# Performance work log

Measured on AMD Instinct MI355X. Metric: run time of the kernel, lower is better.

The kernel has to match this reference:

```python
import jax, jax.numpy as jnp
import numpy as np

N = 50000      # nodes
E = 800000     # edges (avg degree 16)
F_IN = 128     # input features
HID = 64       # hidden per head
HEADS = 4      # heads per layer
G = 256        # graphs in batch
C = 10         # classes
ALPHA = 0.01   # leaky relu negative slope


def setup_inputs() -> dict:
    key = jax.random.key(0)
    ks = jax.random.split(key, 12)
    x = jax.random.normal(ks[0], (N, F_IN), dtype=jnp.float32)
    edge_index = jax.random.randint(ks[1], (2, E), 0, N, dtype=jnp.int32)
    batch = jnp.sort(jax.random.randint(ks[2], (N,), 0, G, dtype=jnp.int32))

    def glorot(k, shape):
        fan_in = shape[0] if len(shape) == 2 else int(np.prod(shape[1:]))
        return (jax.random.normal(k, shape, dtype=jnp.float32) / np.float32(np.sqrt(fan_in)))

    W1 = glorot(ks[3], (F_IN, HEADS * HID))
    a1_src = glorot(ks[4], (HEADS, HID))
    a1_dst = glorot(ks[5], (HEADS, HID))
    W2 = glorot(ks[6], (HEADS * HID, HEADS * HID))
    a2_src = glorot(ks[7], (HEADS, HID))
    a2_dst = glorot(ks[8], (HEADS, HID))
    lin_W = glorot(ks[9], (2 * HEADS * HID, C))
    lin_b = jnp.zeros((C,), dtype=jnp.float32)
    return {
        "x": x, "edge_index": edge_index, "batch": batch,
        "W1": W1, "a1_src": a1_src, "a1_dst": a1_dst,
        "W2": W2, "a2_src": a2_src, "a2_dst": a2_dst,
        "lin_W": lin_W, "lin_b": lin_b,
    }


def _gat_layer(x, src, dst, W, a_src, a_dst):
    """Multi-head GAT layer: edge softmax over incoming neighbors, concat heads, ELU."""
    n = x.shape[0]
    h, f = a_src.shape
    Wh = (x @ W).reshape(n, h, f)                       # [N,H,F]
    # per-node attention logits (decomposed GAT attention a^T [Wh_i || Wh_j])
    ls = jnp.einsum("nhf,hf->nh", Wh, a_src)            # [N,H]
    ld = jnp.einsum("nhf,hf->nh", Wh, a_dst)            # [N,H]
    e = jax.nn.leaky_relu(ls[src] + ld[dst], ALPHA)      # [E,H]
    # numerically-stable softmax over edges grouped by destination node
    m = jax.ops.segment_max(e, dst, num_segments=n)      # [N,H]
    m = jnp.where(jnp.isfinite(m), m, 0.0)
    p = jnp.exp(e - m[dst])                              # [E,H]
    z = jax.ops.segment_sum(p, dst, num_segments=n)      # [N,H]
    attn = p / (z[dst] + 1e-16)                          # [E,H]
    msg = Wh[src] * attn[:, :, None]                     # [E,H,F]
    out = jax.ops.segment_sum(msg, dst, num_segments=n)  # [N,H,F]
    return jax.nn.elu(out.reshape(n, h * f))


def reference(x, edge_index, batch, W1, a1_src, a1_dst, W2, a2_src, a2_dst, lin_W, lin_b):
    src, dst = edge_index[0], edge_index[1]
    x = _gat_layer(x, src, dst, W1, a1_src, a1_dst)
    x = _gat_layer(x, src, dst, W2, a2_src, a2_dst)
    # global max / mean pool per graph
    mx = jax.ops.segment_max(x, batch, num_segments=G)
    mx = jnp.where(jnp.isfinite(mx), mx, 0.0)
    s = jax.ops.segment_sum(x, batch, num_segments=G)
    cnt = jax.ops.segment_sum(jnp.ones((x.shape[0], 1), x.dtype), batch, num_segments=G)
    mean = s / jnp.maximum(cnt, 1.0)
    pooled = jnp.concatenate([mx, mean], axis=1)         # [G, 2*H*F]
    return pooled @ lin_W + lin_b                        # [G, C]
```

## Files before the change

kernel.cpp:

```cpp
#include <hip/hip_runtime.h>
#include <hip/hip_bf16.h>

#define NNODES 50000
#define NEDGES 800000
#define FIN    128
#define HID    64
#define HEADS  4
#define NGRAPH 256
#define NCLS   10
#define DTOT   256
#define ALPHA  0.01f
#define CAPLG  6
#define CAP    (1 << CAPLG)

typedef short bf16x8 __attribute__((ext_vector_type(8)));
typedef float f32x4  __attribute__((ext_vector_type(4)));

#define NB      ((NNODES + 255) / 256)
#define EB      ((NEDGES + 255) / 256)
#define XB      ((NNODES * FIN / 4 + 255) / 256)
#define W1B     (FIN * DTOT / 256)
#define W2B     (DTOT * DTOT / 256)

__device__ __forceinline__ ushort f2bf(float v) {
    return __bfloat16_as_ushort(__float2bfloat16(v));
}
__device__ __forceinline__ float blo(unsigned u) { return __uint_as_float(u << 16); }
__device__ __forceinline__ float bhi(unsigned u) { return __uint_as_float(u & 0xffff0000u); }

__global__ __launch_bounds__(256) void k_setup(const int* __restrict__ src, const int* __restrict__ dst,
                                               int* __restrict__ cursor, ushort* __restrict__ esrc,
                                               const int* __restrict__ batch, int* __restrict__ gstart,
                                               const float4* __restrict__ x4, ushort4* __restrict__ xbf4,
                                               const float* __restrict__ W1, ushort* __restrict__ W1t,
                                               const float* __restrict__ W2, ushort* __restrict__ W2t) {
    int b = blockIdx.x, t = threadIdx.x;
    if (b < EB) {
        int e = b * 256 + t;
        if (e < NEDGES) {
            int d = dst[e];
            int pos = atomicAdd(&cursor[d], 1);
            if (pos < CAP) esrc[(d << CAPLG) + pos] = (ushort)src[e];
        }
    } else if (b < EB + NB) {
        int i = (b - EB) * 256 + t;
        if (i >= NNODES) return;
        int bb = batch[i];
        if (i == 0) {
            for (int g = 0; g <= bb; ++g) gstart[g] = 0;
        } else {
            int pb = batch[i - 1];
            if (pb != bb) for (int g = pb + 1; g <= bb; ++g) gstart[g] = i;
        }
        if (i == NNODES - 1)
            for (int g = bb + 1; g <= NGRAPH; ++g) gstart[g] = NNODES;
    } else if (b < EB + NB + XB) {
        int i = (b - EB - NB) * 256 + t;
        if (i >= NNODES * FIN / 4) return;
        float4 v = x4[i];
        ushort4 o;
        o.x = f2bf(v.x); o.y = f2bf(v.y); o.z = f2bf(v.z); o.w = f2bf(v.w);
        xbf4[i] = o;
    } else if (b < EB + NB + XB + W1B) {
        int id = (b - EB - NB - XB) * 256 + t;
        int n = id & 255, k = id >> 8;
        W1t[n * FIN + (((k >> 3) ^ (n & 7)) << 3) + (k & 7)] = f2bf(W1[k * DTOT + n]);
    } else {
        int id = (b - EB - NB - XB - W1B) * 256 + t;
        int n = id & 255, k = id >> 8;
        W2t[n * DTOT + (((k >> 3) ^ (n & 7)) << 3) + (k & 7)] = f2bf(W2[k * DTOT + n]);
    }
}

template <int K>
__global__ __launch_bounds__(256) void k_gemm_mfma(const ushort* __restrict__ Abf,
                                                   const ushort* __restrict__ Bt,
                                                   ushort* __restrict__ Cbf,
                                                   float* __restrict__ ls,
                                                   float* __restrict__ ld_,
                                                   const float* __restrict__ a_src,
                                                   const float* __restrict__ a_dst,
                                                   int M) {
    __shared__ ushort Bl[128 * K];
    const int tid  = threadIdx.x;
    const int w    = tid >> 6;
    const int lane = tid & 63;
    const int l15  = lane & 15;
    const int quad = lane >> 4;
    const int m0 = blockIdx.y * 128;
    const int n0 = blockIdx.x * 128;
    const int hb = blockIdx.x * 2;

    {
        const uint4* sp = (const uint4*)(Bt + (size_t)n0 * K);
        uint4* dp = (uint4*)Bl;
#pragma unroll
        for (int idx = tid; idx < 128 * K / 8; idx += 256) dp[idx] = sp[idx];
    }
    __syncthreads();

    f32x4 acc[2][8];
#pragma unroll
    for (int mf = 0; mf < 2; ++mf)
#pragma unroll
        for (int nf = 0; nf < 8; ++nf)
            acc[mf][nf] = (f32x4){0.f, 0.f, 0.f, 0.f};

    const int rbase = m0 + w * 32;
    int rowA0 = rbase + l15;       if (rowA0 >= M) rowA0 = M - 1;
    int rowA1 = rbase + 16 + l15;  if (rowA1 >= M) rowA1 = M - 1;
    const ushort* pa0 = Abf + (size_t)rowA0 * K + quad * 8;
    const ushort* pa1 = Abf + (size_t)rowA1 * K + quad * 8;

#pragma unroll
    for (int ks = 0; ks < K / 32; ++ks) {
        bf16x8 a0 = *(const bf16x8*)(pa0 + ks * 32);
        bf16x8 a1 = *(const bf16x8*)(pa1 + ks * 32);
        bf16x8 bfr[8];
#pragma unroll
        for (int nf = 0; nf < 8; ++nf) {
            int n = nf * 16 + l15;
            int c = (ks * 4 + quad) ^ (n & 7);
            bfr[nf] = *(const bf16x8*)&Bl[n * K + (c << 3)];
        }
#pragma unroll
        for (int nf = 0; nf < 8; ++nf) {
            acc[0][nf] = __builtin_amdgcn_mfma_f32_16x16x32_bf16(a0, bfr[nf], acc[0][nf], 0, 0, 0);
            acc[1][nf] = __builtin_amdgcn_mfma_f32_16x16x32_bf16(a1, bfr[nf], acc[1][nf], 0, 0, 0);
        }
    }

    float as[8], ad[8];
#pragma unroll
    for (int nf = 0; nf < 8; ++nf) {
        int head = hb + (nf >> 2);
        as[nf] = a_src[head * HID + (nf & 3) * 16 + l15];
        ad[nf] = a_dst[head * HID + (nf & 3) * 16 + l15];
    }
#pragma unroll
    for (int mf = 0; mf < 2; ++mf) {
#pragma unroll
        for (int reg = 0; reg < 4; ++reg) {
            int row = rbase + mf * 16 + quad * 4 + reg;
            bool ok = row < M;
            if (ok) {
#pragma unroll
                for (int nf = 0; nf < 8; ++nf)
                    Cbf[(size_t)row * DTOT + n0 + nf * 16 + l15] = f2bf(acc[mf][nf][reg]);
            }
            float s0 = 0.f, d0 = 0.f, s1 = 0.f, d1 = 0.f;
#pragma unroll
            for (int nf = 0; nf < 4; ++nf) {
                s0 += acc[mf][nf][reg] * as[nf];
                d0 += acc[mf][nf][reg] * ad[nf];
                s1 += acc[mf][nf + 4][reg] * as[nf + 4];
                d1 += acc[mf][nf + 4][reg] * ad[nf + 4];
            }
#pragma unroll
            for (int off = 1; off < 16; off <<= 1) {
                s0 += __shfl_xor(s0, off);
                d0 += __shfl_xor(d0, off);
                s1 += __shfl_xor(s1, off);
                d1 += __shfl_xor(d1, off);
            }
            if (ok && l15 == 0) {
                ls[row * HEADS + hb]      = s0;
                ld_[row * HEADS + hb]     = d0;
                ls[row * HEADS + hb + 1]  = s1;
                ld_[row * HEADS + hb + 1] = d1;
            }
        }
    }
}

__global__ __launch_bounds__(256) void k_gat_aggr(const int* __restrict__ cnt,
                                                  const ushort* __restrict__ esrc,
                                                  const ushort* __restrict__ Whbf,
                                                  const float* __restrict__ ls,
                                                  const float* __restrict__ ld_,
                                                  ushort* __restrict__ out) {
    const int wv   = threadIdx.x >> 6;
    const int lane = threadIdx.x & 63;
    const int i    = blockIdx.x * 4 + wv;
    if (i >= NNODES) return;
    const int half = lane >> 5;
    const int l32  = lane & 31;
    const int h    = l32 >> 3;
    const int e0 = i << CAPLG;
    int deg = cnt[i]; if (deg > CAP) deg = CAP;
    const int e1 = e0 + deg;
    const float ldv = ld_[i * HEADS + h];

    float mx = -INFINITY;
    for (int e = e0 + (l32 & 7) + 8 * half; e < e1; e += 16)
        mx = fmaxf(mx, ls[(int)esrc[e] * HEADS + h]);
    mx = fmaxf(mx, __shfl_xor(mx, 1));
    mx = fmaxf(mx, __shfl_xor(mx, 2));
    mx = fmaxf(mx, __shfl_xor(mx, 4));
    mx = fmaxf(mx, __shfl_xor(mx, 32));
    float lvm = mx + ldv;
    const float M = lvm > 0.f ? lvm : ALPHA * lvm;

    float ac[8] = {};
    float z = 0.f;
    const int ch = 8 * l32;
    int e = e0 + half;
    for (; e + 6 < e1; e += 8) {
        int s0 = (int)esrc[e], s1 = (int)esrc[e + 2], s2 = (int)esrc[e + 4], s3 = (int)esrc[e + 6];
        float l0 = ls[s0 * HEADS + h] + ldv;
        float l1 = ls[s1 * HEADS + h] + ldv;
        float l2 = ls[s2 * HEADS + h] + ldv;
        float l3 = ls[s3 * HEADS + h] + ldv;
        uint4 u0 = *(const uint4*)&Whbf[(size_t)s0 * DTOT + ch];
        uint4 u1 = *(const uint4*)&Whbf[(size_t)s1 * DTOT + ch];
        uint4 u2 = *(const uint4*)&Whbf[(size_t)s2 * DTOT + ch];
        uint4 u3 = *(const uint4*)&Whbf[(size_t)s3 * DTOT + ch];
        float p0 = __expf((l0 > 0.f ? l0 : ALPHA * l0) - M);
        float p1 = __expf((l1 > 0.f ? l1 : ALPHA * l1) - M);
        float p2 = __expf((l2 > 0.f ? l2 : ALPHA * l2) - M);
        float p3 = __expf((l3 > 0.f ? l3 : ALPHA * l3) - M);
        z += p0 + p1 + p2 + p3;
        ac[0] = fmaf(p0, blo(u0.x), ac[0]); ac[1] = fmaf(p0, bhi(u0.x), ac[1]);
        ac[2] = fmaf(p0, blo(u0.y), ac[2]); ac[3] = fmaf(p0, bhi(u0.y), ac[3]);
        ac[4] = fmaf(p0, blo(u0.z), ac[4]); ac[5] = fmaf(p0, bhi(u0.z), ac[5]);
        ac[6] = fmaf(p0, blo(u0.w), ac[6]); ac[7] = fmaf(p0, bhi(u0.w), ac[7]);
        ac[0] = fmaf(p1, blo(u1.x), ac[0]); ac[1] = fmaf(p1, bhi(u1.x), ac[1]);
        ac[2] = fmaf(p1, blo(u1.y), ac[2]); ac[3] = fmaf(p1, bhi(u1.y), ac[3]);
        ac[4] = fmaf(p1, blo(u1.z), ac[4]); ac[5] = fmaf(p1, bhi(u1.z), ac[5]);
        ac[6] = fmaf(p1, blo(u1.w), ac[6]); ac[7] = fmaf(p1, bhi(u1.w), ac[7]);
        ac[0] = fmaf(p2, blo(u2.x), ac[0]); ac[1] = fmaf(p2, bhi(u2.x), ac[1]);
        ac[2] = fmaf(p2, blo(u2.y), ac[2]); ac[3] = fmaf(p2, bhi(u2.y), ac[3]);
        ac[4] = fmaf(p2, blo(u2.z), ac[4]); ac[5] = fmaf(p2, bhi(u2.z), ac[5]);
        ac[6] = fmaf(p2, blo(u2.w), ac[6]); ac[7] = fmaf(p2, bhi(u2.w), ac[7]);
        ac[0] = fmaf(p3, blo(u3.x), ac[0]); ac[1] = fmaf(p3, bhi(u3.x), ac[1]);
        ac[2] = fmaf(p3, blo(u3.y), ac[2]); ac[3] = fmaf(p3, bhi(u3.y), ac[3]);
        ac[4] = fmaf(p3, blo(u3.z), ac[4]); ac[5] = fmaf(p3, bhi(u3.z), ac[5]);
        ac[6] = fmaf(p3, blo(u3.w), ac[6]); ac[7] = fmaf(p3, bhi(u3.w), ac[7]);
    }
    for (; e < e1; e += 2) {
        int s0 = (int)esrc[e];
        float l0 = ls[s0 * HEADS + h] + ldv;
        uint4 u0 = *(const uint4*)&Whbf[(size_t)s0 * DTOT + ch];
        float p0 = __expf((l0 > 0.f ? l0 : ALPHA * l0) - M);
        z += p0;
        ac[0] = fmaf(p0, blo(u0.x), ac[0]); ac[1] = fmaf(p0, bhi(u0.x), ac[1]);
        ac[2] = fmaf(p0, blo(u0.y), ac[2]); ac[3] = fmaf(p0, bhi(u0.y), ac[3]);
        ac[4] = fmaf(p0, blo(u0.z), ac[4]); ac[5] = fmaf(p0, bhi(u0.z), ac[5]);
        ac[6] = fmaf(p0, blo(u0.w), ac[6]); ac[7] = fmaf(p0, bhi(u0.w), ac[7]);
    }

#pragma unroll
    for (int j = 0; j < 8; ++j) ac[j] += __shfl_xor(ac[j], 32);
    z += __shfl_xor(z, 32);

    if (half == 0) {
        const float inv = 1.f / (z + 1e-16f);
        float v[8];
#pragma unroll
        for (int j = 0; j < 8; ++j) {
            float t = ac[j] * inv;
            v[j] = t > 0.f ? t : __expf(t) - 1.f;
        }
        ushort4 pk, pk2;
        pk.x  = f2bf(v[0]); pk.y  = f2bf(v[1]); pk.z  = f2bf(v[2]); pk.w  = f2bf(v[3]);
        pk2.x = f2bf(v[4]); pk2.y = f2bf(v[5]); pk2.z = f2bf(v[6]); pk2.w = f2bf(v[7]);
        *(ushort4*)(out + (size_t)i * DTOT + ch)     = pk;
        *(ushort4*)(out + (size_t)i * DTOT + ch + 4) = pk2;
    }
}

__global__ __launch_bounds__(1024) void k_pool_final(const ushort* __restrict__ h2bf,
                                                     const int* __restrict__ gstart,
                                                     const float* __restrict__ W,
                                                     const float* __restrict__ b,
                                                     float* __restrict__ out) {
    __shared__ float smx[4][256];
    __shared__ float ssm[4][256];
    __shared__ float pooled[2 * DTOT];
    int g = blockIdx.x, t = threadIdx.x;
    int c = t & 255, j = t >> 8;
    int s = gstart[g], e = gstart[g + 1];
    float mx = -INFINITY, sm = 0.f;
    for (int n = s + j; n < e; n += 4) {
        float vv = __uint_as_float(((unsigned)h2bf[(size_t)n * DTOT + c]) << 16);
        mx = fmaxf(mx, vv);
        sm += vv;
    }
    smx[j][c] = mx;
    ssm[j][c] = sm;
    __syncthreads();
    if (t < 256) {
        float m = fmaxf(fmaxf(smx[0][t], smx[1][t]), fmaxf(smx[2][t], smx[3][t]));
        float su = ssm[0][t] + ssm[1][t] + ssm[2][t] + ssm[3][t];
        int cnt = e - s;
        if (cnt <= 0) m = 0.f;
        pooled[t] = m;
        pooled[DTOT + t] = su / (float)(cnt > 0 ? cnt : 1);
    }
    __syncthreads();
    int wv = t >> 6, lane = t & 63;
    if (wv < NCLS) {
        float acc = 0.f;
        for (int k = lane; k < 2 * DTOT; k += 64)
            acc += pooled[k] * W[k * NCLS + wv];
#pragma unroll
        for (int off = 32; off; off >>= 1) acc += __shfl_down(acc, off);
        if (lane == 0)
            out[g * NCLS + wv] = acc + b[wv];
    }
}

extern "C" void kernel_launch(void* const* d_in, const int* in_sizes, int n_in,
                              void* d_out, int out_size, void* d_ws, size_t ws_size,
                              hipStream_t stream) {
    const float* x     = (const float*)d_in[0];
    const int*   ei    = (const int*)d_in[1];
    const int*   batch = (const int*)d_in[2];
    const float* W1    = (const float*)d_in[3];
    const float* a1s   = (const float*)d_in[4];
    const float* a1d   = (const float*)d_in[5];
    const float* W2    = (const float*)d_in[6];
    const float* a2s   = (const float*)d_in[7];
    const float* a2d   = (const float*)d_in[8];
    const float* linW  = (const float*)d_in[9];
    const float* linb  = (const float*)d_in[10];
    float* out = (float*)d_out;

    const int* src = ei;
    const int* dst = ei + NEDGES;

    size_t off = 0;
    char* base = (char*)d_ws;
    auto alloc = [&](size_t bytes) -> void* {
        void* p = base + off;
        off += (bytes + 255) & ~(size_t)255;
        return p;
    };
    ushort* xbf    = (ushort*)alloc((size_t)NNODES * FIN * 2);
    ushort* Whbf   = (ushort*)alloc((size_t)NNODES * DTOT * 2);
    ushort* h1bf   = (ushort*)alloc((size_t)NNODES * DTOT * 2);
    ushort* h2bf   = (ushort*)alloc((size_t)NNODES * DTOT * 2);
    float*  ls     = (float*)alloc((size_t)NNODES * HEADS * 4);
    float*  ld_    = (float*)alloc((size_t)NNODES * HEADS * 4);
    int*    cursor = (int*)alloc((size_t)NNODES * 4);
    ushort* esrc   = (ushort*)alloc((size_t)(NNODES << CAPLG) * 2);
    int*    gstart = (int*)alloc((size_t)(NGRAPH + 1) * 4);
    ushort* W1t    = (ushort*)alloc((size_t)DTOT * FIN * 2);
    ushort* W2t    = (ushort*)alloc((size_t)DTOT * DTOT * 2);

    hipMemsetAsync(cursor, 0, (size_t)NNODES * 4, stream);

    int setup_blocks = EB + NB + XB + W1B + W2B;
    k_setup<<<setup_blocks, 256, 0, stream>>>(src, dst, cursor, esrc, batch, gstart,
                                              (const float4*)x, (ushort4*)xbf,
                                              W1, W1t, W2, W2t);

    dim3 ggrid(2, (NNODES + 127) / 128);

    k_gemm_mfma<FIN><<<ggrid, 256, 0, stream>>>(xbf, W1t, Whbf, ls, ld_, a1s, a1d, NNODES);
    k_gat_aggr<<<(NNODES + 3) / 4, 256, 0, stream>>>(cursor, esrc, Whbf, ls, ld_, h1bf);

    k_gemm_mfma<DTOT><<<ggrid, 256, 0, stream>>>(h1bf, W2t, Whbf, ls, ld_, a2s, a2d, NNODES);
    k_gat_aggr<<<(NNODES + 3) / 4, 256, 0, stream>>>(cursor, esrc, Whbf, ls, ld_, h2bf);

    k_pool_final<<<NGRAPH, 1024, 0, stream>>>(h2bf, gstart, linW, linb, out);
}
```

Baseline: 320.9 us.

## Compute edge softmax once per lane in LDS and use packed FMA aggregation

The GAT aggregation kernel now has each lane own one incoming edge. Each lane computes the logits for all four heads, and wave shuffles give the max and the sum. The normalized attention weights and source ids go into LDS, which removes the separate max pass and the repeated exp and ls gathers in the main loop. The accumulation uses two-wide float FMAs meant to map to packed FMA instructions, and the output is written as a single 16-byte store. The change adds an early exit for zero-degree nodes and relies on the degree cap equalling the wave size.

New measurement: 324.5 us. Within noise of the previous version (+1.1%).

```diff
diff --git a/kernel.cpp b/kernel.cpp
--- a/kernel.cpp
+++ b/kernel.cpp
@@ -15,6 +15,7 @@
 
 typedef short bf16x8 __attribute__((ext_vector_type(8)));
 typedef float f32x4  __attribute__((ext_vector_type(4)));
+typedef float f32x2  __attribute__((ext_vector_type(2)));
 
 #define NB      ((NNODES + 255) / 256)
 #define EB      ((NEDGES + 255) / 256)
@@ -27,6 +28,12 @@
 }
 __device__ __forceinline__ float blo(unsigned u) { return __uint_as_float(u << 16); }
 __device__ __forceinline__ float bhi(unsigned u) { return __uint_as_float(u & 0xffff0000u); }
+__device__ __forceinline__ f32x2 bfpair(unsigned u) {
+    return (f32x2){__uint_as_float(u << 16), __uint_as_float(u & 0xffff0000u)};
+}
+__device__ __forceinline__ unsigned pack2(float lo, float hi) {
+    return ((unsigned)f2bf(hi) << 16) | (unsigned)f2bf(lo);
+}
 
 __global__ __launch_bounds__(256) void k_setup(const int* __restrict__ src, const int* __restrict__ dst,
                                                int* __restrict__ cursor, ushort* __restrict__ esrc,
@@ -179,6 +186,8 @@
                                                   const float* __restrict__ ls,
                                                   const float* __restrict__ ld_,
                                                   ushort* __restrict__ out) {
+    __shared__ float lds_p[4][CAP][HEADS];
+    __shared__ int   lds_s[4][CAP];
     const int wv   = threadIdx.x >> 6;
     const int lane = threadIdx.x & 63;
     const int i    = blockIdx.x * 4 + wv;
@@ -186,86 +195,123 @@
     const int half = lane >> 5;
     const int l32  = lane & 31;
     const int h    = l32 >> 3;
+    const int ch   = 8 * l32;
+
+    int deg = cnt[i]; if (deg > CAP) deg = CAP;
+
+    if (deg == 0) {
+        if (half == 0) {
+            uint4 zz = {0u, 0u, 0u, 0u};
+            *(uint4*)(out + (size_t)i * DTOT + ch) = zz;
+        }
+        return;
+    }
+
     const int e0 = i << CAPLG;
-    int deg = cnt[i]; if (deg > CAP) deg = CAP;
-    const int e1 = e0 + deg;
-    const float ldv = ld_[i * HEADS + h];
-
-    float mx = -INFINITY;
-    for (int e = e0 + (l32 & 7) + 8 * half; e < e1; e += 16)
-        mx = fmaxf(mx, ls[(int)esrc[e] * HEADS + h]);
-    mx = fmaxf(mx, __shfl_xor(mx, 1));
-    mx = fmaxf(mx, __shfl_xor(mx, 2));
-    mx = fmaxf(mx, __shfl_xor(mx, 4));
-    mx = fmaxf(mx, __shfl_xor(mx, 32));
-    float lvm = mx + ldv;
-    const float M = lvm > 0.f ? lvm : ALPHA * lvm;
-
-    float ac[8] = {};
-    float z = 0.f;
-    const int ch = 8 * l32;
-    int e = e0 + half;
-    for (; e + 6 < e1; e += 8) {
-        int s0 = (int)esrc[e], s1 = (int)esrc[e + 2], s2 = (int)esrc[e + 4], s3 = (int)esrc[e + 6];
-        float l0 = ls[s0 * HEADS + h] + ldv;
-        float l1 = ls[s1 * HEADS + h] + ldv;
-        float l2 = ls[s2 * HEADS + h] + ldv;
-        float l3 = ls[s3 * HEADS + h] + ldv;
+    const bool valid = lane < deg;
+    const int  el = valid ? lane : deg - 1;
+    const int  s  = (int)esrc[e0 + el];
+    const float4 ls4 = *(const float4*)(ls + s * HEADS);
+    const float4 ld4 = *(const float4*)(ld_ + (size_t)i * HEADS);
+
+    float eh[4], mh[4];
+#pragma unroll
+    for (int hh = 0; hh < 4; ++hh) {
+        float v = (&ls4.x)[hh] + (&ld4.x)[hh];
+        v = v > 0.f ? v : ALPHA * v;
+        eh[hh] = valid ? v : -INFINITY;
+        mh[hh] = eh[hh];
+    }
+    for (int off = 1; off < deg; off <<= 1) {
+#pragma unroll
+        for (int hh = 0; hh < 4; ++hh)
+            mh[hh] = fmaxf(mh[hh], __shfl_xor(mh[hh], off));
+    }
+    float ph[4], zh[4];
+#pragma unroll
+    for (int hh = 0; hh < 4; ++hh) {
+        ph[hh] = valid ? __expf(eh[hh] - mh[hh]) : 0.f;
+        zh[hh] = ph[hh];
+    }
+    for (int off = 1; off < deg; off <<= 1) {
+#pragma unroll
+        for (int hh = 0; hh < 4; ++hh)
+            zh[hh] += __shfl_xor(zh[hh], off);
+    }
+#pragma unroll
+    for (int hh = 0; hh < 4; ++hh)
+        ph[hh] *= 1.f / (zh[hh] + 1e-16f);
+
+    *(float4*)&lds_p[wv][lane][0] = make_float4(ph[0], ph[1], ph[2], ph[3]);
+    lds_s[wv][lane] = s;
+
+    f32x2 ac[4];
+#pragma unroll
+    for (int j = 0; j < 4; ++j) ac[j] = (f32x2){0.f, 0.f};
+
+    int e = half;
+    for (; e + 6 < deg; e += 8) {
+        int s0 = lds_s[wv][e];
+        int s1 = lds_s[wv][e + 2];
+        int s2 = lds_s[wv][e + 4];
+        int s3 = lds_s[wv][e + 6];
+        float p0 = lds_p[wv][e][h];
+        float p1 = lds_p[wv][e + 2][h];
+        float p2 = lds_p[wv][e + 4][h];
+        float p3 = lds_p[wv][e + 6][h];
         uint4 u0 = *(const uint4*)&Whbf[(size_t)s0 * DTOT + ch];
         uint4 u1 = *(const uint4*)&Whbf[(size_t)s1 * DTOT + ch];
         uint4 u2 = *(const uint4*)&Whbf[(size_t)s2 * DTOT + ch];
         uint4 u3 = *(const uint4*)&Whbf[(size_t)s3 * DTOT + ch];
-        float p0 = __expf((l0 > 0.f ? l0 : ALPHA * l0) - M);
-        float p1 = __expf((l1 > 0.f ? l1 : ALPHA * l1) - M);
-        float p2 = __expf((l2 > 0.f ? l2 : ALPHA * l2) - M);
-        float p3 = __expf((l3 > 0.f ? l3 : ALPHA * l3) - M);
-        z += p0 + p1 + p2 + p3;
-        ac[0] = fmaf(p0, blo(u0.x), ac[0]); ac[1] = fmaf(p0, bhi(u0.x), ac[1]);
-        ac[2] = fmaf(p0, blo(u0.y), ac[2]); ac[3] = fmaf(p0, bhi(u0.y), ac[3]);
-        ac[4] = fmaf(p0, blo(u0.z), ac[4]); ac[5] = fmaf(p0, bhi(u0.z), ac[5]);
-        ac[6] = fmaf(p0, blo(u0.w), ac[6]); ac[7] = fmaf(p0, bhi(u0.w), ac[7]);
-        ac[0] = fmaf(p1, blo(u1.x), ac[0]); ac[1] = fmaf(p1, bhi(u1.x), ac[1]);
-        ac[2] = fmaf(p1, blo(u1.y), ac[2]); ac[3] = fmaf(p1, bhi(u1.y), ac[3]);
-        ac[4] = fmaf(p1, blo(u1.z), ac[4]); ac[5] = fmaf(p1, bhi(u1.z), ac[5]);
-        ac[6] = fmaf(p1, blo(u1.w), ac[6]); ac[7] = fmaf(p1, bhi(u1.w), ac[7]);
-        ac[0] = fmaf(p2, blo(u2.x), ac[0]); ac[1] = fmaf(p2, bhi(u2.x), ac[1]);
-        ac[2] = fmaf(p2, blo(u2.y), ac[2]); ac[3] = fmaf(p2, bhi(u2.y), ac[3]);
-        ac[4] = fmaf(p2, blo(u2.z), ac[4]); ac[5] = fmaf(p2, bhi(u2.z), ac[5]);
-        ac[6] = fmaf(p2, blo(u2.w), ac[6]); ac[7] = fmaf(p2, bhi(u2.w), ac[7]);
-        ac[0] = fmaf(p3, blo(u3.x), ac[0]); ac[1] = fmaf(p3, bhi(u3.x), ac[1]);
-        ac[2] = fmaf(p3, blo(u3.y), ac[2]); ac[3] = fmaf(p3, bhi(u3.y), ac[3]);
-        ac[4] = fmaf(p3, blo(u3.z), ac[4]); ac[5] = fmaf(p3, bhi(u3.z), ac[5]);
-        ac[6] = fmaf(p3, blo(u3.w), ac[6]); ac[7] = fmaf(p3, bhi(u3.w), ac[7]);
-    }
-    for (; e < e1; e += 2) {
-        int s0 = (int)esrc[e];
-        float l0 = ls[s0 * HEADS + h] + ldv;
+        f32x2 pp0 = {p0, p0}, pp1 = {p1, p1}, pp2 = {p2, p2}, pp3 = {p3, p3};
+        ac[0] = __builtin_elementwise_fma(pp0, bfpair(u0.x), ac[0]);
+        ac[1] = __builtin_elementwise_fma(pp0, bfpair(u0.y), ac[1]);
+        ac[2] = __builtin_elementwise_fma(pp0, bfpair(u0.z), ac[2]);
+        ac[3] = __builtin_elementwise_fma(pp0, bfpair(u0.w), ac[3]);
+        ac[0] = __builtin_elementwise_fma(pp1, bfpair(u1.x), ac[0]);
+        ac[1] = __builtin_elementwise_fma(pp1, bfpair(u1.y), ac[1]);
+        ac[2] = __builtin_elementwise_fma(pp1, bfpair(u1.z), ac[2]);
+        ac[3] = __builtin_elementwise_fma(pp1, bfpair(u1.w), ac[3]);
+        ac[0] = __builtin_elementwise_fma(pp2, bfpair(u2.x), ac[0]);
+        ac[1] = __builtin_elementwise_fma(pp2, bfpair(u2.y), ac[1]);
+        ac[2] = __builtin_elementwise_fma(pp2, bfpair(u2.z), ac[2]);
+        ac[3] = __builtin_elementwise_fma(pp2, bfpair(u2.w), ac[3]);
+        ac[0] = __builtin_elementwise_fma(pp3, bfpair(u3.x), ac[0]);
+        ac[1] = __builtin_elementwise_fma(pp3, bfpair(u3.y), ac[1]);
+        ac[2] = __builtin_elementwise_fma(pp3, bfpair(u3.z), ac[2]);
+        ac[3] = __builtin_elementwise_fma(pp3, bfpair(u3.w), ac[3]);
+    }
+    for (; e < deg; e += 2) {
+        int s0 = lds_s[wv][e];
+        float p0 = lds_p[wv][e][h];
         uint4 u0 = *(const uint4*)&Whbf[(size_t)s0 * DTOT + ch];
-        float p0 = __expf((l0 > 0.f ? l0 : ALPHA * l0) - M);
-        z += p0;
-        ac[0] = fmaf(p0, blo(u0.x), ac[0]); ac[1] = fmaf(p0, bhi(u0.x), ac[1]);
-        ac[2] = fmaf(p0, blo(u0.y), ac[2]); ac[3] = fmaf(p0, bhi(u0.y), ac[3]);
-        ac[4] = fmaf(p0, blo(u0.z), ac[4]); ac[5] = fmaf(p0, bhi(u0.z), ac[5]);
-        ac[6] = fmaf(p0, blo(u0.w), ac[6]); ac[7] = fmaf(p0, bhi(u0.w), ac[7]);
-    }
-
-#pragma unroll
-    for (int j = 0; j < 8; ++j) ac[j] += __shfl_xor(ac[j], 32);
-    z += __shfl_xor(z, 32);
+        f32x2 pp0 = {p0, p0};
+        ac[0] = __builtin_elementwise_fma(pp0, bfpair(u0.x), ac[0]);
+        ac[1] = __builtin_elementwise_fma(pp0, bfpair(u0.y), ac[1]);
+        ac[2] = __builtin_elementwise_fma(pp0, bfpair(u0.z), ac[2]);
+        ac[3] = __builtin_elementwise_fma(pp0, bfpair(u0.w), ac[3]);
+    }
+
+#pragma unroll
+    for (int j = 0; j < 4; ++j) {
+        ac[j][0] += __shfl_xor(ac[j][0], 32);
+        ac[j][1] += __shfl_xor(ac[j][1], 32);
+    }
 
     if (half == 0) {
-        const float inv = 1.f / (z + 1e-16f);
         float v[8];
 #pragma unroll
-        for (int j = 0; j < 8; ++j) {
-            float t = ac[j] * inv;
-            v[j] = t > 0.f ? t : __expf(t) - 1.f;
-        }
-        ushort4 pk, pk2;
-        pk.x  = f2bf(v[0]); pk.y  = f2bf(v[1]); pk.z  = f2bf(v[2]); pk.w  = f2bf(v[3]);
-        pk2.x = f2bf(v[4]); pk2.y = f2bf(v[5]); pk2.z = f2bf(v[6]); pk2.w = f2bf(v[7]);
-        *(ushort4*)(out + (size_t)i * DTOT + ch)     = pk;
-        *(ushort4*)(out + (size_t)i * DTOT + ch + 4) = pk2;
+        for (int j = 0; j < 4; ++j) {
+            float t0 = ac[j][0], t1 = ac[j][1];
+            v[2 * j]     = t0 > 0.f ? t0 : __expf(t0) - 1.f;
+            v[2 * j + 1] = t1 > 0.f ? t1 : __expf(t1) - 1.f;
+        }
+        uint4 pk;
+        pk.x = pack2(v[0], v[1]);
+        pk.y = pack2(v[2], v[3]);
+        pk.z = pack2(v[4], v[5]);
+        pk.w = pack2(v[6], v[7]);
+        *(uint4*)(out + (size_t)i * DTOT + ch) = pk;
     }
 }
 
```

## Retile GEMM to full-width N with K-chunked LDS staging; vectorize pooling

Applied to the files above, without the earlier changes.

The GEMM now has each block cover all 256 output columns for 128 rows, using 8 waves that each own 16 rows. The B matrix is staged through LDS in 64-wide K chunks with an XOR swizzle, so each A row is read once instead of twice, and all four heads' attention logits are reduced in one pass. The pooling kernel reads 8 bf16 values per thread with 16-byte loads and spreads nodes over 32 row groups. The cost is extra LDS syncs per K chunk and higher register pressure, since each thread holds 16 accumulators. Pooling also uses more shared memory. The code relies on blo/bhi helpers that presumably exist in the unseen part of the file.

Measured after the change: 319.2 us. About the same (-0.5%).

```diff
diff --git a/kernel.cpp b/kernel.cpp
--- a/kernel.cpp
+++ b/kernel.cpp
@@ -73,7 +73,7 @@
 }
 
 template <int K>
-__global__ __launch_bounds__(256) void k_gemm_mfma(const ushort* __restrict__ Abf,
+__global__ __launch_bounds__(512) void k_gemm_mfma(const ushort* __restrict__ Abf,
                                                    const ushort* __restrict__ Bt,
                                                    ushort* __restrict__ Cbf,
                                                    float* __restrict__ ls,
@@ -81,93 +81,93 @@
                                                    const float* __restrict__ a_src,
                                                    const float* __restrict__ a_dst,
                                                    int M) {
-    __shared__ ushort Bl[128 * K];
+    __shared__ ushort Bl[256 * 64];
     const int tid  = threadIdx.x;
     const int w    = tid >> 6;
     const int lane = tid & 63;
     const int l15  = lane & 15;
     const int quad = lane >> 4;
-    const int m0 = blockIdx.y * 128;
-    const int n0 = blockIdx.x * 128;
-    const int hb = blockIdx.x * 2;
-
-    {
-        const uint4* sp = (const uint4*)(Bt + (size_t)n0 * K);
-        uint4* dp = (uint4*)Bl;
-#pragma unroll
-        for (int idx = tid; idx < 128 * K / 8; idx += 256) dp[idx] = sp[idx];
-    }
-    __syncthreads();
-
-    f32x4 acc[2][8];
-#pragma unroll
-    for (int mf = 0; mf < 2; ++mf)
-#pragma unroll
-        for (int nf = 0; nf < 8; ++nf)
-            acc[mf][nf] = (f32x4){0.f, 0.f, 0.f, 0.f};
-
-    const int rbase = m0 + w * 32;
-    int rowA0 = rbase + l15;       if (rowA0 >= M) rowA0 = M - 1;
-    int rowA1 = rbase + 16 + l15;  if (rowA1 >= M) rowA1 = M - 1;
+    const int m0 = blockIdx.x * 128;
+
+    f32x4 acc[16];
+#pragma unroll
+    for (int nf = 0; nf < 16; ++nf) acc[nf] = (f32x4){0.f, 0.f, 0.f, 0.f};
+
+    int rowA0 = m0 + w * 16 + l15;  if (rowA0 >= M) rowA0 = M - 1;
     const ushort* pa0 = Abf + (size_t)rowA0 * K + quad * 8;
-    const ushort* pa1 = Abf + (size_t)rowA1 * K + quad * 8;
-
-#pragma unroll
-    for (int ks = 0; ks < K / 32; ++ks) {
-        bf16x8 a0 = *(const bf16x8*)(pa0 + ks * 32);
-        bf16x8 a1 = *(const bf16x8*)(pa1 + ks * 32);
-        bf16x8 bfr[8];
-#pragma unroll
-        for (int nf = 0; nf < 8; ++nf) {
-            int n = nf * 16 + l15;
-            int c = (ks * 4 + quad) ^ (n & 7);
-            bfr[nf] = *(const bf16x8*)&Bl[n * K + (c << 3)];
-        }
-#pragma unroll
-        for (int nf = 0; nf < 8; ++nf) {
-            acc[0][nf] = __builtin_amdgcn_mfma_f32_16x16x32_bf16(a0, bfr[nf], acc[0][nf], 0, 0, 0);
-            acc[1][nf] = __builtin_amdgcn_mfma_f32_16x16x32_bf16(a1, bfr[nf], acc[1][nf], 0, 0, 0);
-        }
-    }
-
-    float as[8], ad[8];
-#pragma unroll
-    for (int nf = 0; nf < 8; ++nf) {
-        int head = hb + (nf >> 2);
+
+#pragma unroll
+    for (int kc = 0; kc < K / 64; ++kc) {
+        {
+#pragma unroll
+            for (int idx = tid; idx < 2048; idx += 512) {
+                int n = idx >> 3, c8 = (idx ^ n) & 7;
+                *(uint4*)&Bl[n * 64 + c8 * 8] =
+                    *(const uint4*)&Bt[(size_t)n * K + kc * 64 + c8 * 8];
+            }
+        }
+        __syncthreads();
+#pragma unroll
+        for (int ks = 0; ks < 2; ++ks) {
+            bf16x8 a0 = *(const bf16x8*)(pa0 + kc * 64 + ks * 32);
+#pragma unroll
+            for (int nh = 0; nh < 4; ++nh) {
+                bf16x8 bfr[4];
+#pragma unroll
+                for (int j = 0; j < 4; ++j) {
+                    int n = (nh * 4 + j) * 16 + l15;
+                    int c = (ks * 4 + quad) ^ (n & 7);
+                    bfr[j] = *(const bf16x8*)&Bl[n * 64 + (c << 3)];
+                }
+#pragma unroll
+                for (int j = 0; j < 4; ++j)
+                    acc[nh * 4 + j] = __builtin_amdgcn_mfma_f32_16x16x32_bf16(a0, bfr[j], acc[nh * 4 + j], 0, 0, 0);
+            }
+        }
+        __syncthreads();
+    }
+
+    float as[16], ad[16];
+#pragma unroll
+    for (int nf = 0; nf < 16; ++nf) {
+        int head = nf >> 2;
         as[nf] = a_src[head * HID + (nf & 3) * 16 + l15];
         ad[nf] = a_dst[head * HID + (nf & 3) * 16 + l15];
     }
 #pragma unroll
-    for (int mf = 0; mf < 2; ++mf) {
-#pragma unroll
-        for (int reg = 0; reg < 4; ++reg) {
-            int row = rbase + mf * 16 + quad * 4 + reg;
-            bool ok = row < M;
-            if (ok) {
-#pragma unroll
-                for (int nf = 0; nf < 8; ++nf)
-                    Cbf[(size_t)row * DTOT + n0 + nf * 16 + l15] = f2bf(acc[mf][nf][reg]);
-            }
-            float s0 = 0.f, d0 = 0.f, s1 = 0.f, d1 = 0.f;
-#pragma unroll
-            for (int nf = 0; nf < 4; ++nf) {
-                s0 += acc[mf][nf][reg] * as[nf];
-                d0 += acc[mf][nf][reg] * ad[nf];
-                s1 += acc[mf][nf + 4][reg] * as[nf + 4];
-                d1 += acc[mf][nf + 4][reg] * ad[nf + 4];
-            }
-#pragma unroll
-            for (int off = 1; off < 16; off <<= 1) {
-                s0 += __shfl_xor(s0, off);
-                d0 += __shfl_xor(d0, off);
-                s1 += __shfl_xor(s1, off);
-                d1 += __shfl_xor(d1, off);
-            }
-            if (ok && l15 == 0) {
-                ls[row * HEADS + hb]      = s0;
-                ld_[row * HEADS + hb]     = d0;
-                ls[row * HEADS + hb + 1]  = s1;
-                ld_[row * HEADS + hb + 1] = d1;
+    for (int reg = 0; reg < 4; ++reg) {
+        int row = m0 + w * 16 + quad * 4 + reg;
+        bool ok = row < M;
+        if (ok) {
+#pragma unroll
+            for (int nf = 0; nf < 16; ++nf)
+                Cbf[(size_t)row * DTOT + nf * 16 + l15] = f2bf(acc[nf][reg]);
+        }
+        float sh[4], dh[4];
+#pragma unroll
+        for (int head = 0; head < 4; ++head) {
+            float s = 0.f, d = 0.f;
+#pragma unroll
+            for (int j = 0; j < 4; ++j) {
+                int nf = head * 4 + j;
+                s += acc[nf][reg] * as[nf];
+                d += acc[nf][reg] * ad[nf];
+            }
+            sh[head] = s; dh[head] = d;
+        }
+#pragma unroll
+        for (int off = 1; off < 16; off <<= 1) {
+#pragma unroll
+            for (int head = 0; head < 4; ++head) {
+                sh[head] += __shfl_xor(sh[head], off);
+                dh[head] += __shfl_xor(dh[head], off);
+            }
+        }
+        if (ok && l15 == 0) {
+#pragma unroll
+            for (int head = 0; head < 4; ++head) {
+                ls[row * HEADS + head]  = sh[head];
+                ld_[row * HEADS + head] = dh[head];
             }
         }
     }
@@ -274,31 +274,55 @@
                                                      const float* __restrict__ W,
                                                      const float* __restrict__ b,
                                                      float* __restrict__ out) {
-    __shared__ float smx[4][256];
-    __shared__ float ssm[4][256];
+    __shared__ float smx[16][256];
+    __shared__ float ssm[16][256];
     __shared__ float pooled[2 * DTOT];
     int g = blockIdx.x, t = threadIdx.x;
-    int c = t & 255, j = t >> 8;
+    int cg = t & 31, j = t >> 5;
     int s = gstart[g], e = gstart[g + 1];
-    float mx = -INFINITY, sm = 0.f;
-    for (int n = s + j; n < e; n += 4) {
-        float vv = __uint_as_float(((unsigned)h2bf[(size_t)n * DTOT + c]) << 16);
-        mx = fmaxf(mx, vv);
-        sm += vv;
-    }
-    smx[j][c] = mx;
-    ssm[j][c] = sm;
+    float mx[8], sm[8];
+#pragma unroll
+    for (int k = 0; k < 8; ++k) { mx[k] = -INFINITY; sm[k] = 0.f; }
+    for (int n = s + j; n < e; n += 32) {
+        uint4 u = *(const uint4*)&h2bf[(size_t)n * DTOT + cg * 8];
+        float v0 = blo(u.x), v1 = bhi(u.x), v2 = blo(u.y), v3 = bhi(u.y);
+        float v4 = blo(u.z), v5 = bhi(u.z), v6 = blo(u.w), v7 = bhi(u.w);
+        mx[0] = fmaxf(mx[0], v0); sm[0] += v0;
+        mx[1] = fmaxf(mx[1], v1); sm[1] += v1;
+        mx[2] = fmaxf(mx[2], v2); sm[2] += v2;
+        mx[3] = fmaxf(mx[3], v3); sm[3] += v3;
+        mx[4] = fmaxf(mx[4], v4); sm[4] += v4;
+        mx[5] = fmaxf(mx[5], v5); sm[5] += v5;
+        mx[6] = fmaxf(mx[6], v6); sm[6] += v6;
+        mx[7] = fmaxf(mx[7], v7); sm[7] += v7;
+    }
+#pragma unroll
+    for (int k = 0; k < 8; ++k) {
+        mx[k] = fmaxf(mx[k], __shfl_xor(mx[k], 32));
+        sm[k] += __shfl_xor(sm[k], 32);
+    }
+    int wave = t >> 6, lane = t & 63;
+    if (lane < 32) {
+        *(float4*)&smx[wave][lane * 8]     = make_float4(mx[0], mx[1], mx[2], mx[3]);
+        *(float4*)&smx[wave][lane * 8 + 4] = make_float4(mx[4], mx[5], mx[6], mx[7]);
+        *(float4*)&ssm[wave][lane * 8]     = make_float4(sm[0], sm[1], sm[2], sm[3]);
+        *(float4*)&ssm[wave][lane * 8 + 4] = make_float4(sm[4], sm[5], sm[6], sm[7]);
+    }
     __syncthreads();
     if (t < 256) {
-        float m = fmaxf(fmaxf(smx[0][t], smx[1][t]), fmaxf(smx[2][t], smx[3][t]));
-        float su = ssm[0][t] + ssm[1][t] + ssm[2][t] + ssm[3][t];
+        float m = -INFINITY, su = 0.f;
+#pragma unroll
+        for (int jj = 0; jj < 16; ++jj) {
+            m = fmaxf(m, smx[jj][t]);
+            su += ssm[jj][t];
+        }
         int cnt = e - s;
         if (cnt <= 0) m = 0.f;
         pooled[t] = m;
         pooled[DTOT + t] = su / (float)(cnt > 0 ? cnt : 1);
     }
     __syncthreads();
-    int wv = t >> 6, lane = t & 63;
+    int wv = t >> 6;
     if (wv < NCLS) {
         float acc = 0.f;
         for (int k = lane; k < 2 * DTOT; k += 64)
@@ -355,12 +379,12 @@
                                               (const float4*)x, (ushort4*)xbf,
                                               W1, W1t, W2, W2t);
 
-    dim3 ggrid(2, (NNODES + 127) / 128);
-
-    k_gemm_mfma<FIN><<<ggrid, 256, 0, stream>>>(xbf, W1t, Whbf, ls, ld_, a1s, a1d, NNODES);
+    int ggrid = (NNODES + 127) / 128;
+
+    k_gemm_mfma<FIN><<<ggrid, 512, 0, stream>>>(xbf, W1t, Whbf, ls, ld_, a1s, a1d, NNODES);
     k_gat_aggr<<<(NNODES + 3) / 4, 256, 0, stream>>>(cursor, esrc, Whbf, ls, ld_, h1bf);
 
-    k_gemm_mfma<DTOT><<<ggrid, 256, 0, stream>>>(h1bf, W2t, Whbf, ls, ld_, a2s, a2d, NNODES);
+    k_gemm_mfma<DTOT><<<ggrid, 512, 0, stream>>>(h1bf, W2t, Whbf, ls, ld_, a2s, a2d, NNODES);
     k_gat_aggr<<<(NNODES + 3) / 4, 256, 0, stream>>>(cursor, esrc, Whbf, ls, ld_, h2bf);
 
     k_pool_final<<<NGRAPH, 1024, 0, stream>>>(h2bf, gstart, linW, linb, out);
```
